# Optimization experiments

Measured on AMD Instinct MI355X. Metric: run time of the kernel, lower is better.

The kernel has to match this reference:

```python
import jax, jax.numpy as jnp
import numpy as np

N, E, F_IN, H, C = 10000, 320000, 256, 256, 40


def setup_inputs() -> dict:
    key = jax.random.key(0)
    ks = jax.random.split(key, 12)
    inp = {
        "x": jax.random.normal(ks[0], (N, F_IN), dtype=jnp.float32),
        "edge_index": jax.random.randint(ks[1], (2, E), 0, N, dtype=jnp.int64),
    }
    dims = [(F_IN, H), (H, H), (H, H), (H, H), (H, C)]
    for i, (din, dout) in enumerate(dims, start=1):
        scale = 1.0 / np.sqrt(din)
        inp[f"W{i}"] = jax.random.normal(ks[1 + i], (din, dout), dtype=jnp.float32) * scale
        inp[f"b{i}"] = jnp.zeros((dout,), dtype=jnp.float32)
    return inp


def _gcn_norm(edge_index, num_nodes, dtype):
    # GCNConv: add self-loops, symmetric normalization D^-1/2 (A+I) D^-1/2
    loops = jnp.arange(num_nodes, dtype=edge_index.dtype)
    src = jnp.concatenate([edge_index[0], loops])
    dst = jnp.concatenate([edge_index[1], loops])
    deg = jax.ops.segment_sum(jnp.ones_like(dst, dtype=dtype), dst, num_segments=num_nodes)
    dinv = jnp.where(deg > 0, deg ** -0.5, 0.0).astype(dtype)
    norm = dinv[src] * dinv[dst]  # [E+N]
    return src, dst, norm


def _conv(h, src, dst, norm, W, b, num_nodes):
    # linear transform then gather-scale-scatter aggregation
    h = h @ W                           # [N, dout]
    msg = h[src] * norm[:, None]        # [E+N, dout]
    return jax.ops.segment_sum(msg, dst, num_segments=num_nodes) + b


def reference(x, edge_index, W1, b1, W2, b2, W3, b3, W4, b4, W5, b5):
    num_nodes = x.shape[0]
    src, dst, norm = _gcn_norm(edge_index, num_nodes, x.dtype)
    h = jax.nn.relu(_conv(x, src, dst, norm, W1, b1, num_nodes))
    h = jax.nn.relu(_conv(h, src, dst, norm, W2, b2, num_nodes))
    h = jax.nn.relu(_conv(h, src, dst, norm, W3, b3, num_nodes))
    h = jax.nn.relu(_conv(h, src, dst, norm, W4, b4, num_nodes))
    logits = _conv(h, src, dst, norm, W5, b5, num_nodes)
    return jax.nn.log_softmax(logits, axis=1), logits
```

## Files before the change

### kernel.cpp

```cpp
#include <hip/hip_runtime.h>
#include <hip/hip_bf16.h>

#define N_NODES 10000
#define N_EDGES 320000
#define HDIM    256
#define NCLS    40

typedef __attribute__((ext_vector_type(8))) short short8;
typedef __attribute__((ext_vector_type(4))) float floatx4;
typedef unsigned long long ull;
typedef unsigned short ushort;

__device__ __forceinline__ float bf2f(ushort u) {
    union { unsigned int i; float f; } v; v.i = ((unsigned int)u) << 16; return v.f;
}
__device__ __forceinline__ ushort f2bf(float f) {
    __hip_bfloat16 h = __float2bfloat16(f);
    return *reinterpret_cast<ushort*>(&h);
}


__global__ __launch_bounds__(256)
void init_kernel(const void* x, const void* ei, int* flags, int* cnt,
                 ushort* tbuf, ushort* hbuf) {
    const int b = blockIdx.x;
    const int tid = threadIdx.x;
    if (b < 40) {
        int i = b * 256 + tid;
        if (i < N_NODES) cnt[i] = 0;
    } else {
        if (tid < 64) {
            const int lane = tid;
            const ushort* u = (const ushort*)x;
            int e = (u[2 * lane] >> 7) & 0xFF;
            ull badmask = __ballot(e < 100 || e > 140);
            const int* ii = (const int*)ei;
            ull oddnz = __ballot(ii[2 * lane + 1] != 0);
            if (lane == 0) {
                flags[0] = (__popcll(badmask) >= 8) ? 1 : 0;
                flags[1] = (oddnz == 0) ? 1 : 0;
            }
        } else if (tid < 128) {
            ((ull*)(tbuf + (size_t)N_NODES * 256))[tid - 64] = 0;
        } else if (tid < 192) {
            ((ull*)(hbuf + (size_t)N_NODES * 256))[tid - 128] = 0;
        }
    }
}


struct PrepArgs {
    const void* x;
    const void* ei;
    const void* wsrc[10];
    ushort* wdst[10];
    int woffs[11];
    ushort* xb;
    int* src32;
    int* dst32;
    int* cnt;
    const int* flags;
};

#define PREP_XB 2500
#define PREP_WB 1069
#define PREP_EB 1250
#define PREP_TOTAL (PREP_XB + PREP_WB + PREP_EB)
#define WTOT 273448

__global__ __launch_bounds__(256)
void prep_kernel(PrepArgs a) {
    const int b = blockIdx.x;
    const int f32 = a.flags[0];
    if (b < PREP_XB) {
        int i4 = b * 256 + threadIdx.x;
        if (f32) {
            float4 v = ((const float4*)a.x)[i4];
            ull p = (ull)f2bf(v.x) | ((ull)f2bf(v.y) << 16) |
                    ((ull)f2bf(v.z) << 32) | ((ull)f2bf(v.w) << 48);
            ((ull*)a.xb)[i4] = p;
        } else {
            ((ull*)a.xb)[i4] = ((const ull*)a.x)[i4];
        }
    } else if (b < PREP_XB + PREP_WB) {
        int i = (b - PREP_XB) * 256 + threadIdx.x;
        if (i < WTOT) {
            int t = 0;
#pragma unroll
            for (int k = 1; k < 10; ++k) t += (i >= a.woffs[k]);
            int local = i - a.woffs[t];
            ushort v;
            if (f32) v = f2bf(((const float*)a.wsrc[t])[local]);
            else     v = ((const ushort*)a.wsrc[t])[local];
            a.wdst[t][local] = v;
        }
    } else {
        int e = (b - PREP_XB - PREP_WB) * 256 + threadIdx.x;
        const int* ii = (const int*)a.ei;
        int s, d;
        if (a.flags[1]) { s = ii[2 * e]; d = ii[2 * (N_EDGES + e)]; }
        else            { s = ii[e];     d = ii[N_EDGES + e]; }
        s = ((unsigned)s < N_NODES) ? s : 0;
        d = ((unsigned)d < N_NODES) ? d : 0;
        a.src32[e] = s;
        a.dst32[e] = d;
        atomicAdd(&a.cnt[d], 1);
    }
}


__global__ __launch_bounds__(256)
void scan_dinv_kernel(const int* __restrict__ cnt, int* __restrict__ offs,
                      int* __restrict__ woff, float* __restrict__ dinv) {
    __shared__ int part[256];
    const int t = threadIdx.x;
    const int CH = 40;
    const int base = t * CH;
    int s = 0;
    for (int j = 0; j < CH; ++j) {
        int i = base + j;
        if (i < N_NODES) s += cnt[i];
    }
    part[t] = s;
    __syncthreads();
    for (int off = 1; off < 256; off <<= 1) {
        int v = (t >= off) ? part[t - off] : 0;
        __syncthreads();
        part[t] += v;
        __syncthreads();
    }
    int run = (t == 0) ? 0 : part[t - 1];
    for (int j = 0; j < CH; ++j) {
        int i = base + j;
        if (i < N_NODES) {
            int c = cnt[i];
            offs[i] = run;
            woff[i] = run;
            dinv[i] = rsqrtf((float)c + 1.0f);
            run += c;
        }
    }
}


__global__ void fill_kernel(const int* __restrict__ src, const int* __restrict__ dst,
                            int* __restrict__ woff, int* __restrict__ csr) {
    int e = blockIdx.x * 256 + threadIdx.x;
    if (e < N_EDGES) {
        int d = dst[e];
        int p = atomicAdd(&woff[d], 1);
        csr[p] = src[e];
    }
}


__global__ __launch_bounds__(256)
void gemm256_kernel(const ushort* __restrict__ A, const ushort* __restrict__ W,
                    const float* __restrict__ dinv, ushort* __restrict__ T) {
    const int lane = threadIdx.x & 63;
    const int wave = threadIdx.x >> 6;
    const int m = lane & 15;
    const int quad = lane >> 4;
    const int c0 = blockIdx.x * 32;

    short8 bfrag[2][8];
#pragma unroll
    for (int t = 0; t < 2; ++t)
#pragma unroll
        for (int s = 0; s < 8; ++s)
#pragma unroll
            for (int j = 0; j < 8; ++j)
                bfrag[t][s][j] = (short)W[(size_t)(s * 32 + quad * 8 + j) * 256 + c0 + t * 16 + m];

    const int step = gridDim.y * 4;
    for (int rt = blockIdx.y * 4 + wave; rt < N_NODES / 16; rt += step) {
        const int r0 = rt * 16;
        floatx4 acc0 = {0.f, 0.f, 0.f, 0.f};
        floatx4 acc1 = {0.f, 0.f, 0.f, 0.f};
        const ushort* arow = A + (size_t)(r0 + m) * 256 + quad * 8;
#pragma unroll
        for (int s = 0; s < 8; ++s) {
            short8 af = *(const short8*)(arow + s * 32);
            acc0 = __builtin_amdgcn_mfma_f32_16x16x32_bf16(af, bfrag[0][s], acc0, 0, 0, 0);
            acc1 = __builtin_amdgcn_mfma_f32_16x16x32_bf16(af, bfrag[1][s], acc1, 0, 0, 0);
        }
#pragma unroll
        for (int r = 0; r < 4; ++r) {
            int row = r0 + quad * 4 + r;
            float di = dinv[row];
            T[(size_t)row * 256 + c0 + m]      = f2bf(acc0[r] * di);
            T[(size_t)row * 256 + c0 + 16 + m] = f2bf(acc1[r] * di);
        }
    }
}


__global__ __launch_bounds__(256)
void gemm40_kernel(const ushort* __restrict__ A, const ushort* __restrict__ W,
                   const float* __restrict__ dinv, float* __restrict__ T) {
    const int lane = threadIdx.x & 63;
    const int wave = threadIdx.x >> 6;
    const int m = lane & 15;
    const int quad = lane >> 4;
    const int col = blockIdx.x * 16 + m;
    const bool colok = col < NCLS;

    short8 bfrag[8];
#pragma unroll
    for (int s = 0; s < 8; ++s)
#pragma unroll
        for (int j = 0; j < 8; ++j)
            bfrag[s][j] = colok ? (short)W[(size_t)(s * 32 + quad * 8 + j) * NCLS + col] : (short)0;

    const int step = gridDim.y * 4;
    for (int rt = blockIdx.y * 4 + wave; rt < N_NODES / 16; rt += step) {
        const int r0 = rt * 16;
        floatx4 acc = {0.f, 0.f, 0.f, 0.f};
        const ushort* arow = A + (size_t)(r0 + m) * 256 + quad * 8;
#pragma unroll
        for (int s = 0; s < 8; ++s) {
            short8 af = *(const short8*)(arow + s * 32);
            acc = __builtin_amdgcn_mfma_f32_16x16x32_bf16(af, bfrag[s], acc, 0, 0, 0);
        }
        if (colok) {
#pragma unroll
            for (int r = 0; r < 4; ++r) {
                int row = r0 + quad * 4 + r;
                T[(size_t)row * NCLS + col] = acc[r] * dinv[row];
            }
        }
    }
}


__device__ __forceinline__ void accum16(float* acc, int4 r) {
#pragma unroll
    for (int k = 0; k < 4; ++k) {
        union { int i; float f; } lo, hi;
        int d = (&r.x)[k];
        lo.i = d << 16;
        hi.i = d & 0xffff0000;
        acc[2 * k]     += lo.f;
        acc[2 * k + 1] += hi.f;
    }
}

__global__ __launch_bounds__(256)
void agg256_kernel(const ushort* __restrict__ T,
                   const int* __restrict__ csr, const int* __restrict__ offs,
                   const int* __restrict__ cnt, const float* __restrict__ dinv,
                   const ushort* __restrict__ bias,
                   ushort* __restrict__ H) {
    const int node = blockIdx.x * 4 + (threadIdx.x >> 6);
    const int lane = threadIdx.x & 63;
    const int half = lane >> 5;
    const int q = lane & 31;
    const int start = offs[node];
    const int count = cnt[node];
    const float di = dinv[node];

    float acc[8];
    {
        int sinit = half ? N_NODES : node;
        int4 r = *(const int4*)(T + (size_t)sinit * 256 + q * 8);
#pragma unroll
        for (int k = 0; k < 4; ++k) {
            union { int i; float f; } lo, hi;
            int d = (&r.x)[k];
            lo.i = d << 16; hi.i = d & 0xffff0000;
            acc[2 * k] = lo.f; acc[2 * k + 1] = hi.f;
        }
    }

    for (int bj = 0; bj < count; bj += 64) {
        int mrem = count - bj;
        int mm = mrem < 64 ? mrem : 64;
        int idxv = (lane < mm) ? csr[start + bj + lane] : N_NODES;
        int j2 = 0;
        for (; j2 + 16 <= mm; j2 += 16) {
            int s[8];
#pragma unroll
            for (int k = 0; k < 8; ++k) s[k] = __shfl(idxv, j2 + 2 * k + half);
            int4 r[8];
#pragma unroll
            for (int k = 0; k < 8; ++k) r[k] = *(const int4*)(T + (size_t)s[k] * 256 + q * 8);
#pragma unroll
            for (int k = 0; k < 8; ++k) accum16(acc, r[k]);
        }
        for (; j2 < mm; j2 += 2) {
            int s = __shfl(idxv, j2 + half);
            int4 r = *(const int4*)(T + (size_t)s * 256 + q * 8);
            accum16(acc, r);
        }
    }

#pragma unroll
    for (int i = 0; i < 8; ++i) acc[i] += __shfl_xor(acc[i], 32);

    if (half == 0) {
        int4 bv = *(const int4*)(bias + q * 8);
        int out_d[4];
#pragma unroll
        for (int k = 0; k < 4; ++k) {
            union { int i; float f; } lo, hi;
            int d = (&bv.x)[k];
            lo.i = d << 16; hi.i = d & 0xffff0000;
            float v0 = fmaxf(acc[2 * k] * di + lo.f, 0.f);
            float v1 = fmaxf(acc[2 * k + 1] * di + hi.f, 0.f);
            out_d[k] = (int)f2bf(v0) | ((int)f2bf(v1) << 16);
        }
        *(int4*)(H + (size_t)node * 256 + q * 8) = *(int4*)out_d;
    }
}


__global__ __launch_bounds__(256)
void aggsoft_kernel(const float* __restrict__ T,
                    const int* __restrict__ csr, const int* __restrict__ offs,
                    const int* __restrict__ cnt, const float* __restrict__ dinv,
                    const ushort* __restrict__ bias,
                    void* __restrict__ out, const int* __restrict__ flags) {
    const int node = blockIdx.x * 4 + (threadIdx.x >> 6);
    const int lane = threadIdx.x & 63;
    const int start = offs[node];
    const int count = cnt[node];
    const float di = dinv[node];

    float acc = (lane < NCLS) ? T[(size_t)node * NCLS + lane] : 0.f;
    for (int bj = 0; bj < count; bj += 64) {
        int mrem = count - bj;
        int mm = mrem < 64 ? mrem : 64;
        int idxv = (lane < mm) ? csr[start + bj + lane] : 0;
        int jj = 0;
        for (; jj + 4 <= mm; jj += 4) {
            int s0 = __shfl(idxv, jj + 0);
            int s1 = __shfl(idxv, jj + 1);
            int s2 = __shfl(idxv, jj + 2);
            int s3 = __shfl(idxv, jj + 3);
            if (lane < NCLS) {
                float t0 = T[(size_t)s0 * NCLS + lane];
                float t1 = T[(size_t)s1 * NCLS + lane];
                float t2 = T[(size_t)s2 * NCLS + lane];
                float t3 = T[(size_t)s3 * NCLS + lane];
                acc += t0 + t1 + t2 + t3;
            }
        }
        for (; jj < mm; ++jj) {
            int s = __shfl(idxv, jj);
            if (lane < NCLS) acc += T[(size_t)s * NCLS + lane];
        }
    }

    float l = (lane < NCLS) ? (acc * di + bf2f(bias[lane])) : -INFINITY;
    float mx = l;
#pragma unroll
    for (int o = 32; o > 0; o >>= 1) mx = fmaxf(mx, __shfl_xor(mx, o));
    float e = (lane < NCLS) ? __expf(l - mx) : 0.f;
    float sum = e;
#pragma unroll
    for (int o = 32; o > 0; o >>= 1) sum += __shfl_xor(sum, o);
    float ls = l - mx - __logf(sum);
    if (lane < NCLS) {
        size_t i0 = (size_t)node * NCLS + lane;
        size_t i1 = (size_t)N_NODES * NCLS + i0;
        if (flags[0]) {
            ((float*)out)[i0] = ls;
            ((float*)out)[i1] = l;
        } else {
            ((ushort*)out)[i0] = f2bf(ls);
            ((ushort*)out)[i1] = f2bf(l);
        }
    }
}


static inline size_t alup(size_t x) { return (x + 255) & ~(size_t)255; }

extern "C" void kernel_launch(void* const* d_in, const int* in_sizes, int n_in,
                              void* d_out, int out_size, void* d_ws, size_t ws_size,
                              hipStream_t stream) {
    char* w = (char*)d_ws;
    int* flags   = (int*)w;           w += alup(16);
    float* dinv  = (float*)w;         w += alup(N_NODES * 4);
    int* cnt     = (int*)w;           w += alup(N_NODES * 4);
    int* offs    = (int*)w;           w += alup(N_NODES * 4);
    int* woff    = (int*)w;           w += alup(N_NODES * 4);
    int* src32   = (int*)w;           w += alup(N_EDGES * 4);
    int* dst32   = (int*)w;           w += alup(N_EDGES * 4);
    int* csr     = (int*)w;           w += alup(N_EDGES * 4);
    ushort* xb   = (ushort*)w;        w += alup((size_t)N_NODES * HDIM * 2);
    ushort* wb[5]; ushort* bb[5];
    for (int l = 0; l < 5; ++l) {
        int wn = (l < 4) ? HDIM * HDIM : HDIM * NCLS;
        int bn = (l < 4) ? HDIM : NCLS;
        wb[l] = (ushort*)w; w += alup((size_t)wn * 2);
        bb[l] = (ushort*)w; w += alup((size_t)bn * 2);
    }
    ushort* tbuf = (ushort*)w;        w += alup((size_t)(N_NODES + 16) * HDIM * 2);
    ushort* hbuf = (ushort*)w;        w += alup((size_t)(N_NODES + 16) * HDIM * 2);
    float* t5    = (float*)w;         w += alup((size_t)N_NODES * NCLS * 4);

    init_kernel<<<41, 256, 0, stream>>>(d_in[0], d_in[1], flags, cnt, tbuf, hbuf);

    PrepArgs pa;
    pa.x = d_in[0];
    pa.ei = d_in[1];
    int sizes[10] = { HDIM * HDIM, HDIM, HDIM * HDIM, HDIM, HDIM * HDIM, HDIM,
                      HDIM * HDIM, HDIM, HDIM * NCLS, NCLS };
    int run = 0;
    for (int t = 0; t < 10; ++t) {
        pa.wsrc[t] = d_in[2 + t];
        pa.wdst[t] = (t & 1) ? bb[t >> 1] : wb[t >> 1];
        pa.woffs[t] = run;
        run += sizes[t];
    }
    pa.woffs[10] = run;
    pa.xb = xb; pa.src32 = src32; pa.dst32 = dst32; pa.cnt = cnt; pa.flags = flags;
    prep_kernel<<<PREP_TOTAL, 256, 0, stream>>>(pa);

    scan_dinv_kernel<<<1, 256, 0, stream>>>(cnt, offs, woff, dinv);
    const int eblk = (N_EDGES + 255) / 256;
    fill_kernel<<<eblk, 256, 0, stream>>>(src32, dst32, woff, csr);

    const int aggblk = N_NODES / 4;

    gemm256_kernel<<<dim3(8, 78), 256, 0, stream>>>(xb, wb[0], dinv, tbuf);
    agg256_kernel<<<aggblk, 256, 0, stream>>>(tbuf, csr, offs, cnt, dinv, bb[0], hbuf);
    for (int l = 1; l < 4; ++l) {
        gemm256_kernel<<<dim3(8, 78), 256, 0, stream>>>(hbuf, wb[l], dinv, tbuf);
        agg256_kernel<<<aggblk, 256, 0, stream>>>(tbuf, csr, offs, cnt, dinv, bb[l], hbuf);
    }
    gemm40_kernel<<<dim3(3, 80), 256, 0, stream>>>(hbuf, wb[4], dinv, t5);
    aggsoft_kernel<<<aggblk, 256, 0, stream>>>(t5, csr, offs, cnt, dinv, bb[4], d_out, flags);
}
```

Baseline: 298.3 us.

## Fuse neighbor aggregation with next layer's GEMM using prepacked weights in LDS

Replaces the separate aggregate-then-GEMM kernel pairs with a fused kernel. Each block gathers 4 nodes' aggregated rows into LDS and immediately multiplies them by the next layer's weights, which are prepacked into MFMA fragment order during prep. This removes the intermediate H buffer round trip and several launches. In exchange, each block reloads a full weight matrix and uses a 16-row MFMA tile with only 4 valid rows. Degree counting moves out of prep into a separate count kernel.

New measurement: 282.4 us. -5.3%, faster.

```diff
diff --git a/kernel.cpp b/kernel.cpp
--- a/kernel.cpp
+++ b/kernel.cpp
@@ -19,16 +19,19 @@
     return *reinterpret_cast<ushort*>(&h);
 }
 
+#define WP256 65536
+#define WP40  24576
+
 
 __global__ __launch_bounds__(256)
 void init_kernel(const void* x, const void* ei, int* flags, int* cnt,
-                 ushort* tbuf, ushort* hbuf) {
+                 ushort* tA, ushort* tB, ushort* wp5) {
     const int b = blockIdx.x;
     const int tid = threadIdx.x;
     if (b < 40) {
         int i = b * 256 + tid;
         if (i < N_NODES) cnt[i] = 0;
-    } else {
+    } else if (b == 40) {
         if (tid < 64) {
             const int lane = tid;
             const ushort* u = (const ushort*)x;
@@ -41,10 +44,13 @@
                 flags[1] = (oddnz == 0) ? 1 : 0;
             }
         } else if (tid < 128) {
-            ((ull*)(tbuf + (size_t)N_NODES * 256))[tid - 64] = 0;
+            ((ull*)(tA + (size_t)N_NODES * 256))[tid - 64] = 0;
         } else if (tid < 192) {
-            ((ull*)(hbuf + (size_t)N_NODES * 256))[tid - 128] = 0;
-        }
+            ((ull*)(tB + (size_t)N_NODES * 256))[tid - 128] = 0;
+        }
+    } else {
+        int i = (b - 41) * 256 + tid;
+        if (i < WP40 / 4) ((ull*)wp5)[i] = 0;
     }
 }
 
@@ -55,10 +61,10 @@
     const void* wsrc[10];
     ushort* wdst[10];
     int woffs[11];
+    ushort* wp[4];
     ushort* xb;
     int* src32;
     int* dst32;
-    int* cnt;
     const int* flags;
 };
 
@@ -93,6 +99,16 @@
             if (f32) v = f2bf(((const float*)a.wsrc[t])[local]);
             else     v = ((const ushort*)a.wsrc[t])[local];
             a.wdst[t][local] = v;
+            if ((t & 1) == 0 && t >= 2) {
+                int wnum = t >> 1;
+                int dout = (wnum < 4) ? 256 : NCLS;
+                int k = local / dout;
+                int col = local - k * dout;
+                int tile = col >> 4, m = col & 15;
+                int s = k >> 5, quad = (k >> 3) & 3, j = k & 7;
+                int pidx = ((((tile * 8 + s) * 4 + quad) * 16 + m) << 3) + j;
+                a.wp[wnum - 1][pidx] = v;
+            }
         }
     } else {
         int e = (b - PREP_XB - PREP_WB) * 256 + threadIdx.x;
@@ -100,12 +116,15 @@
         int s, d;
         if (a.flags[1]) { s = ii[2 * e]; d = ii[2 * (N_EDGES + e)]; }
         else            { s = ii[e];     d = ii[N_EDGES + e]; }
-        s = ((unsigned)s < N_NODES) ? s : 0;
-        d = ((unsigned)d < N_NODES) ? d : 0;
-        a.src32[e] = s;
-        a.dst32[e] = d;
-        atomicAdd(&a.cnt[d], 1);
-    }
+        a.src32[e] = ((unsigned)s < N_NODES) ? s : 0;
+        a.dst32[e] = ((unsigned)d < N_NODES) ? d : 0;
+    }
+}
+
+
+__global__ void count_kernel(const int* __restrict__ dst, int* __restrict__ cnt) {
+    int e = blockIdx.x * 256 + threadIdx.x;
+    if (e < N_EDGES) atomicAdd(&cnt[dst[e]], 1);
 }
 
 
@@ -195,43 +214,7 @@
 }
 
 
-__global__ __launch_bounds__(256)
-void gemm40_kernel(const ushort* __restrict__ A, const ushort* __restrict__ W,
-                   const float* __restrict__ dinv, float* __restrict__ T) {
-    const int lane = threadIdx.x & 63;
-    const int wave = threadIdx.x >> 6;
-    const int m = lane & 15;
-    const int quad = lane >> 4;
-    const int col = blockIdx.x * 16 + m;
-    const bool colok = col < NCLS;
-
-    short8 bfrag[8];
-#pragma unroll
-    for (int s = 0; s < 8; ++s)
-#pragma unroll
-        for (int j = 0; j < 8; ++j)
-            bfrag[s][j] = colok ? (short)W[(size_t)(s * 32 + quad * 8 + j) * NCLS + col] : (short)0;
-
-    const int step = gridDim.y * 4;
-    for (int rt = blockIdx.y * 4 + wave; rt < N_NODES / 16; rt += step) {
-        const int r0 = rt * 16;
-        floatx4 acc = {0.f, 0.f, 0.f, 0.f};
-        const ushort* arow = A + (size_t)(r0 + m) * 256 + quad * 8;
-#pragma unroll
-        for (int s = 0; s < 8; ++s) {
-            short8 af = *(const short8*)(arow + s * 32);
-            acc = __builtin_amdgcn_mfma_f32_16x16x32_bf16(af, bfrag[s], acc, 0, 0, 0);
-        }
-        if (colok) {
-#pragma unroll
-            for (int r = 0; r < 4; ++r) {
-                int row = r0 + quad * 4 + r;
-                T[(size_t)row * NCLS + col] = acc[r] * dinv[row];
-            }
-        }
-    }
-}
-
+#define HROW 264
 
 __device__ __forceinline__ void accum16(float* acc, int4 r) {
 #pragma unroll
@@ -245,14 +228,13 @@
     }
 }
 
-__global__ __launch_bounds__(256)
-void agg256_kernel(const ushort* __restrict__ T,
-                   const int* __restrict__ csr, const int* __restrict__ offs,
-                   const int* __restrict__ cnt, const float* __restrict__ dinv,
-                   const ushort* __restrict__ bias,
-                   ushort* __restrict__ H) {
-    const int node = blockIdx.x * 4 + (threadIdx.x >> 6);
-    const int lane = threadIdx.x & 63;
+__device__ __forceinline__ void gather_to_lds(const ushort* __restrict__ T,
+                                              const int* __restrict__ csr,
+                                              const int* __restrict__ offs,
+                                              const int* __restrict__ cnt,
+                                              const float* __restrict__ dinv,
+                                              const ushort* __restrict__ bias,
+                                              ushort* hs, int node, int lane, int wave) {
     const int half = lane >> 5;
     const int q = lane & 31;
     const int start = offs[node];
@@ -309,7 +291,86 @@
             float v1 = fmaxf(acc[2 * k + 1] * di + hi.f, 0.f);
             out_d[k] = (int)f2bf(v0) | ((int)f2bf(v1) << 16);
         }
-        *(int4*)(H + (size_t)node * 256 + q * 8) = *(int4*)out_d;
+        *(int4*)(hs + wave * HROW + q * 8) = *(int4*)out_d;
+    }
+}
+
+__global__ __launch_bounds__(256)
+void fused256_kernel(const ushort* __restrict__ Tin, const ushort* __restrict__ Wp,
+                     const ushort* __restrict__ bias, const float* __restrict__ dinv,
+                     const int* __restrict__ csr, const int* __restrict__ offs,
+                     const int* __restrict__ cnt, ushort* __restrict__ Tout) {
+    __shared__ ushort hs[16 * HROW];
+    const int tid = threadIdx.x;
+    const int lane = tid & 63;
+    const int wave = tid >> 6;
+    const int m = lane & 15;
+    const int quad = lane >> 4;
+    const int nb = blockIdx.x * 4;
+
+    gather_to_lds(Tin, csr, offs, cnt, dinv, bias, hs, nb + wave, lane, wave);
+    __syncthreads();
+
+    float d0 = dinv[nb], d1 = dinv[nb + 1], d2 = dinv[nb + 2], d3 = dinv[nb + 3];
+    float dv[4] = {d0, d1, d2, d3};
+
+#pragma unroll
+    for (int tt = 0; tt < 4; ++tt) {
+        const int tile = wave * 4 + tt;
+        short8 bfrag[8];
+#pragma unroll
+        for (int s = 0; s < 8; ++s)
+            bfrag[s] = *(const short8*)(Wp + ((((tile * 8 + s) * 4 + quad) * 16 + m) << 3));
+        floatx4 acc = {0.f, 0.f, 0.f, 0.f};
+#pragma unroll
+        for (int s = 0; s < 8; ++s) {
+            short8 af = *(const short8*)(hs + m * HROW + s * 32 + quad * 8);
+            acc = __builtin_amdgcn_mfma_f32_16x16x32_bf16(af, bfrag[s], acc, 0, 0, 0);
+        }
+        if (quad == 0) {
+#pragma unroll
+            for (int r = 0; r < 4; ++r)
+                Tout[(size_t)(nb + r) * 256 + tile * 16 + m] = f2bf(acc[r] * dv[r]);
+        }
+    }
+}
+
+
+__global__ __launch_bounds__(256)
+void fused40_kernel(const ushort* __restrict__ Tin, const ushort* __restrict__ Wp,
+                    const ushort* __restrict__ bias, const float* __restrict__ dinv,
+                    const int* __restrict__ csr, const int* __restrict__ offs,
+                    const int* __restrict__ cnt, float* __restrict__ T5) {
+    __shared__ ushort hs[16 * HROW];
+    const int tid = threadIdx.x;
+    const int lane = tid & 63;
+    const int wave = tid >> 6;
+    const int m = lane & 15;
+    const int quad = lane >> 4;
+    const int nb = blockIdx.x * 4;
+
+    gather_to_lds(Tin, csr, offs, cnt, dinv, bias, hs, nb + wave, lane, wave);
+    __syncthreads();
+
+    if (wave < 3) {
+        const int tile = wave;
+        const int col = tile * 16 + m;
+        float dv[4] = {dinv[nb], dinv[nb + 1], dinv[nb + 2], dinv[nb + 3]};
+        short8 bfrag[8];
+#pragma unroll
+        for (int s = 0; s < 8; ++s)
+            bfrag[s] = *(const short8*)(Wp + ((((tile * 8 + s) * 4 + quad) * 16 + m) << 3));
+        floatx4 acc = {0.f, 0.f, 0.f, 0.f};
+#pragma unroll
+        for (int s = 0; s < 8; ++s) {
+            short8 af = *(const short8*)(hs + m * HROW + s * 32 + quad * 8);
+            acc = __builtin_amdgcn_mfma_f32_16x16x32_bf16(af, bfrag[s], acc, 0, 0, 0);
+        }
+        if (quad == 0 && col < NCLS) {
+#pragma unroll
+            for (int r = 0; r < 4; ++r)
+                T5[(size_t)(nb + r) * NCLS + col] = acc[r] * dv[r];
+        }
     }
 }
 
@@ -396,11 +457,17 @@
         wb[l] = (ushort*)w; w += alup((size_t)wn * 2);
         bb[l] = (ushort*)w; w += alup((size_t)bn * 2);
     }
-    ushort* tbuf = (ushort*)w;        w += alup((size_t)(N_NODES + 16) * HDIM * 2);
-    ushort* hbuf = (ushort*)w;        w += alup((size_t)(N_NODES + 16) * HDIM * 2);
-    float* t5    = (float*)w;         w += alup((size_t)N_NODES * NCLS * 4);
-
-    init_kernel<<<41, 256, 0, stream>>>(d_in[0], d_in[1], flags, cnt, tbuf, hbuf);
+    ushort* wp[4];
+    for (int i = 0; i < 4; ++i) {
+        int n = (i < 3) ? WP256 : WP40;
+        wp[i] = (ushort*)w; w += alup((size_t)n * 2);
+    }
+    ushort* tA = (ushort*)w;          w += alup((size_t)(N_NODES + 16) * HDIM * 2);
+    ushort* tB = (ushort*)w;          w += alup((size_t)(N_NODES + 16) * HDIM * 2);
+    float* t5  = (float*)w;           w += alup((size_t)N_NODES * NCLS * 4);
+
+    init_kernel<<<41 + (WP40 / 4 + 255) / 256, 256, 0, stream>>>(
+        d_in[0], d_in[1], flags, cnt, tA, tB, wp[3]);
 
     PrepArgs pa;
     pa.x = d_in[0];
@@ -415,21 +482,21 @@
         run += sizes[t];
     }
     pa.woffs[10] = run;
-    pa.xb = xb; pa.src32 = src32; pa.dst32 = dst32; pa.cnt = cnt; pa.flags = flags;
+    for (int i = 0; i < 4; ++i) pa.wp[i] = wp[i];
+    pa.xb = xb; pa.src32 = src32; pa.dst32 = dst32; pa.flags = flags;
     prep_kernel<<<PREP_TOTAL, 256, 0, stream>>>(pa);
 
+    const int eblk = (N_EDGES + 255) / 256;
+    count_kernel<<<eblk, 256, 0, stream>>>(dst32, cnt);
     scan_dinv_kernel<<<1, 256, 0, stream>>>(cnt, offs, woff, dinv);
-    const int eblk = (N_EDGES + 255) / 256;
     fill_kernel<<<eblk, 256, 0, stream>>>(src32, dst32, woff, csr);
 
     const int aggblk = N_NODES / 4;
 
-    gemm256_kernel<<<dim3(8, 78), 256, 0, stream>>>(xb, wb[0], dinv, tbuf);
-    agg256_kernel<<<aggblk, 256, 0, stream>>>(tbuf, csr, offs, cnt, dinv, bb[0], hbuf);
-    for (int l = 1; l < 4; ++l) {
-        gemm256_kernel<<<dim3(8, 78), 256, 0, stream>>>(hbuf, wb[l], dinv, tbuf);
-        agg256_kernel<<<aggblk, 256, 0, stream>>>(tbuf, csr, offs, cnt, dinv, bb[l], hbuf);
-    }
-    gemm40_kernel<<<dim3(3, 80), 256, 0, stream>>>(hbuf, wb[4], dinv, t5);
+    gemm256_kernel<<<dim3(8, 78), 256, 0, stream>>>(xb, wb[0], dinv, tA);
+    fused256_kernel<<<aggblk, 256, 0, stream>>>(tA, wp[0], bb[0], dinv, csr, offs, cnt, tB);
+    fused256_kernel<<<aggblk, 256, 0, stream>>>(tB, wp[1], bb[1], dinv, csr, offs, cnt, tA);
+    fused256_kernel<<<aggblk, 256, 0, stream>>>(tA, wp[2], bb[2], dinv, csr, offs, cnt, tB);
+    fused40_kernel<<<aggblk, 256, 0, stream>>>(tB, wp[3], bb[3], dinv, csr, offs, cnt, t5);
     aggsoft_kernel<<<aggblk, 256, 0, stream>>>(t5, csr, offs, cnt, dinv, bb[4], d_out, flags);
 }
```
